# Performance work log

Measured on AMD Instinct MI355X. Metric: run time of the kernel, lower is better.

The kernel has to match this reference:

```python
import jax, jax.numpy as jnp
import numpy as np
import math

B, L, D, H = 2, 2048, 512, 8
DH = D // H  # 64
MAX_SEQ = 2048


def setup_inputs() -> dict:
    key = jax.random.key(0)
    ks = jax.random.split(key, 9)
    rn = lambda k, sh: jax.random.normal(k, sh, dtype=jnp.float32)
    w_scale = 0.02
    # causal mask: 1 where attention is disallowed (upper triangle)
    causal = jnp.triu(jnp.ones((L, L), jnp.float32), k=1)[None, None]
    return {
        "q_in": rn(ks[0], (B, L, D)),
        "k_in": rn(ks[1], (B, L, D)),
        "v_in": rn(ks[2], (B, L, D)),
        "mask": causal,
        "Wq": rn(ks[3], (D, D)) * w_scale,
        "bq": jnp.zeros((D,), jnp.float32),
        "Wk": rn(ks[4], (D, D)) * w_scale,
        "bk": jnp.zeros((D,), jnp.float32),
        "Wv": rn(ks[5], (D, D)) * w_scale,
        "bv": jnp.zeros((D,), jnp.float32),
        "Wfc": rn(ks[6], (D, D)) * w_scale,
        "bfc": jnp.zeros((D,), jnp.float32),
        "E": rn(ks[7], (MAX_SEQ, DH)),  # relative position embedding (non-trainable buffer)
    }


def _heads(x, W, b):
    # [B,L,D] -> [B,H,L,DH]
    y = x @ W + b
    return y.reshape(x.shape[0], x.shape[1], H, DH).transpose(0, 2, 1, 3)


def _qe_mask(len_q):
    # keep[l, m] = (m >= len_q - 1 - l); zeros out invalid relative offsets
    rows = jnp.arange(len_q)[:, None]
    cols = jnp.arange(len_q)[None, :]
    return (cols >= (len_q - 1 - rows)).astype(jnp.float32)


def _skew(QE):
    # Music-Transformer skewing: [B,H,L,M] -> pad left on last dim ->
    # reshape swapping last two dims -> drop first row => Srel [B,H,M,L]
    b, h, l, m = QE.shape
    padded = jnp.pad(QE, ((0, 0), (0, 0), (0, 0), (1, 0)))  # [b,h,l,m+1]
    reshaped = padded.reshape(b, h, m + 1, l)
    return reshaped[:, :, 1:, :]  # [b,h,m,l]


def reference(q_in, k_in, v_in, mask, Wq, bq, Wk, bk, Wv, bv, Wfc, bfc, E):
    q = _heads(q_in, Wq, bq)  # [B,H,L,DH]
    k = _heads(k_in, Wk, bk)
    v = _heads(v_in, Wv, bv)
    len_q = q.shape[2]
    # left embedding slice: E[max(0, MAX_SEQ - len_q):]
    e = E[max(0, MAX_SEQ - len_q):, :]  # [M, DH], M == len_q here
    QE = jnp.einsum('bhld,md->bhlm', q, e)
    QE = QE * _qe_mask(len_q)  # broadcast [L,M] over [B,H,L,M]
    Srel = _skew(QE)  # [B,H,L,L]
    QKt = jnp.einsum('bhld,bhmd->bhlm', q, k)
    logits = (QKt + Srel) / np.sqrt(DH).astype(np.float32)
    logits = logits + mask * (-1e9)
    attn_weights = jax.nn.softmax(logits, axis=-1)
    attn = jnp.einsum('bhlm,bhmd->bhld', attn_weights, v)
    out = attn.transpose(0, 2, 1, 3).reshape(q_in.shape[0], -1, D)
    out = out @ Wfc + bfc
    return out, attn_weights
```

## Files before the change

kernel.cpp:

```cpp
#include <hip/hip_runtime.h>
#include <math.h>

#define L 2048
#define DMODEL 512
#define NH 8
#define DH 64
#define NROWS 4096

typedef __attribute__((ext_vector_type(4))) float f32x4;
typedef __attribute__((ext_vector_type(8))) short s16x8;

#define MFMA(a, b, c) __builtin_amdgcn_mfma_f32_16x16x32_bf16(a, b, c, 0, 0, 0)

static __device__ __forceinline__ ushort f2b(float f) {
    union { float f; unsigned u; } v; v.f = f;
    unsigned r = v.u + 0x7FFF + ((v.u >> 16) & 1);
    return (ushort)(r >> 16);
}

__global__ __launch_bounds__(256)
void cvt_bf16(const float* __restrict__ in, ushort* __restrict__ out, int n8) {
    int i = blockIdx.x * 256 + threadIdx.x;
    if (i < n8) {
        float4 a = *reinterpret_cast<const float4*>(&in[(size_t)i * 8]);
        float4 b = *reinterpret_cast<const float4*>(&in[(size_t)i * 8 + 4]);
        ushort4 o0; o0.x = f2b(a.x); o0.y = f2b(a.y); o0.z = f2b(a.z); o0.w = f2b(a.w);
        ushort4 o1; o1.x = f2b(b.x); o1.y = f2b(b.y); o1.z = f2b(b.z); o1.w = f2b(b.w);
        *reinterpret_cast<ushort4*>(&out[(size_t)i * 8]) = o0;
        *reinterpret_cast<ushort4*>(&out[(size_t)i * 8 + 4]) = o1;
    }
}

__global__ __launch_bounds__(256)
void transpose_w(const float* __restrict__ W0, const float* __restrict__ W1,
                 const float* __restrict__ W2, const float* __restrict__ W3,
                 ushort* __restrict__ T0, ushort* __restrict__ T1,
                 ushort* __restrict__ T2, ushort* __restrict__ T3) {
    const int z = blockIdx.z;
    const float* W = z == 0 ? W0 : (z == 1 ? W1 : (z == 2 ? W2 : W3));
    ushort* T = z == 0 ? T0 : (z == 1 ? T1 : (z == 2 ? T2 : T3));
    __shared__ float Ls[64][65];
    const int tid = threadIdx.x;
    const int k0 = blockIdx.y * 64, n0 = blockIdx.x * 64;
    #pragma unroll
    for (int i = 0; i < 4; ++i) {
        int kk = (tid >> 4) + i * 16, n4 = (tid & 15) * 4;
        float4 v = *reinterpret_cast<const float4*>(&W[(size_t)(k0 + kk) * 512 + n0 + n4]);
        Ls[kk][n4] = v.x; Ls[kk][n4 + 1] = v.y; Ls[kk][n4 + 2] = v.z; Ls[kk][n4 + 3] = v.w;
    }
    __syncthreads();
    #pragma unroll
    for (int i = 0; i < 4; ++i) {
        int nn = (tid >> 4) + i * 16, k4 = (tid & 15) * 4;
        ushort4 o;
        o.x = f2b(Ls[k4 + 0][nn]); o.y = f2b(Ls[k4 + 1][nn]);
        o.z = f2b(Ls[k4 + 2][nn]); o.w = f2b(Ls[k4 + 3][nn]);
        *reinterpret_cast<ushort4*>(&T[(size_t)(n0 + nn) * 512 + k0 + k4]) = o;
    }
}

__global__ __launch_bounds__(256)
void gemm_bf16(const void* __restrict__ A0, const void* __restrict__ A1,
               const void* __restrict__ A2,
               const ushort* __restrict__ W0, const ushort* __restrict__ W1,
               const ushort* __restrict__ W2,
               const float* __restrict__ b0, const float* __restrict__ b1,
               const float* __restrict__ b2,
               void* o0, void* o1, void* o2, int a_f32, int modes) {
    const int z = blockIdx.z;
    const void* A   = z == 0 ? A0 : (z == 1 ? A1 : A2);
    const ushort* Wt = z == 0 ? W0 : (z == 1 ? W1 : W2);
    const float* bias = z == 0 ? b0 : (z == 1 ? b1 : b2);
    void* outp = z == 0 ? o0 : (z == 1 ? o1 : o2);
    const int mode = (modes >> (4 * z)) & 15;

    __shared__ ushort As[128][40];
    __shared__ ushort Bs[64][40];
    const int tid = threadIdx.x;
    const int w = tid >> 6, lane = tid & 63, g = lane >> 4, c = lane & 15;
    const int m0 = blockIdx.y * 128, n0 = blockIdx.x * 64;

    f32x4 acc[2][4];
    #pragma unroll
    for (int rs = 0; rs < 2; ++rs)
        #pragma unroll
        for (int cs = 0; cs < 4; ++cs) acc[rs][cs] = (f32x4){0.f, 0.f, 0.f, 0.f};

    float bsv[4];
    #pragma unroll
    for (int cs = 0; cs < 4; ++cs) bsv[cs] = bias[n0 + 16 * cs + c];

    for (int k0 = 0; k0 < 512; k0 += 32) {
        {
            int row = tid >> 1, kh = (tid & 1) * 16;
            if (a_f32) {
                const float* p = (const float*)A + (size_t)(m0 + row) * 512 + k0 + kh;
                ushort tmp[16];
                #pragma unroll
                for (int q4 = 0; q4 < 4; ++q4) {
                    float4 f = *reinterpret_cast<const float4*>(p + q4 * 4);
                    tmp[q4 * 4 + 0] = f2b(f.x); tmp[q4 * 4 + 1] = f2b(f.y);
                    tmp[q4 * 4 + 2] = f2b(f.z); tmp[q4 * 4 + 3] = f2b(f.w);
                }
                *reinterpret_cast<uint4*>(&As[row][kh]) = *reinterpret_cast<uint4*>(&tmp[0]);
                *reinterpret_cast<uint4*>(&As[row][kh + 8]) = *reinterpret_cast<uint4*>(&tmp[8]);
            } else {
                const ushort* p = (const ushort*)A + (size_t)(m0 + row) * 512 + k0 + kh;
                uint4 x0 = *reinterpret_cast<const uint4*>(p);
                uint4 x1 = *reinterpret_cast<const uint4*>(p + 8);
                *reinterpret_cast<uint4*>(&As[row][kh]) = x0;
                *reinterpret_cast<uint4*>(&As[row][kh + 8]) = x1;
            }
        }
        {
            int n = tid >> 2, kh = (tid & 3) * 8;
            uint4 x = *reinterpret_cast<const uint4*>(&Wt[(size_t)(n0 + n) * 512 + k0 + kh]);
            *reinterpret_cast<uint4*>(&Bs[n][kh]) = x;
        }
        __syncthreads();
        s16x8 af[2], bf[4];
        #pragma unroll
        for (int rs = 0; rs < 2; ++rs)
            af[rs] = *reinterpret_cast<const s16x8*>(&As[32 * w + 16 * rs + c][8 * g]);
        #pragma unroll
        for (int cs = 0; cs < 4; ++cs)
            bf[cs] = *reinterpret_cast<const s16x8*>(&Bs[16 * cs + c][8 * g]);
        #pragma unroll
        for (int rs = 0; rs < 2; ++rs)
            #pragma unroll
            for (int cs = 0; cs < 4; ++cs)
                acc[rs][cs] = MFMA(af[rs], bf[cs], acc[rs][cs]);
        __syncthreads();
    }
    #pragma unroll
    for (int rs = 0; rs < 2; ++rs)
        #pragma unroll
        for (int cs = 0; cs < 4; ++cs)
            #pragma unroll
            for (int r = 0; r < 4; ++r) {
                int row = m0 + 32 * w + 16 * rs + 4 * g + r;
                int n = n0 + 16 * cs + c;
                float v = acc[rs][cs][r] + bsv[cs];
                int bb = row >> 11, l = row & 2047, hh = n >> 6, dh = n & 63;
                if (mode == 0) {
                    ((float*)outp)[(size_t)row * 512 + n] = v;
                } else if (mode == 1) {
                    ((ushort*)outp)[(((size_t)bb * NH + hh) * L + l) * DH + dh] = f2b(v);
                } else {
                    ((ushort*)outp)[(((size_t)bb * NH + hh) * DH + dh) * L + l] = f2b(v);
                }
            }
}

__global__ __launch_bounds__(256, 4)
void attn(const ushort* __restrict__ qws, const ushort* __restrict__ kws,
          const ushort* __restrict__ vtg, const ushort* __restrict__ Ebf,
          float* __restrict__ attnw, ushort* __restrict__ ows) {
    __shared__ float Wsc[4][32][68];
    __shared__ float lred[4][32];
    __shared__ float linvs[32];

    const int tid = threadIdx.x;
    const int w = tid >> 6, lane = tid & 63, g = lane >> 4, c = lane & 15;
    const int bid = blockIdx.x;
    const int bh = bid & 15;
    const int ib = 63 - (bid >> 4);
    const int b = bh >> 3, h = bh & 7;
    const int i0 = ib * 32;
    const int nt = ib + 1;

    const ushort* qb = qws + (size_t)bh * L * DH;
    const ushort* kb = kws + (size_t)bh * L * DH;
    const ushort* vt = vtg + (size_t)bh * DH * L;
    float* ab = attnw + (size_t)bh * L * L;

    float*  Ps = &Wsc[w][0][0];
    ushort* Pw = (ushort*)(Ps + 32 * 36);

    s16x8 aq[2][2];
    #pragma unroll
    for (int rs = 0; rs < 2; ++rs)
        #pragma unroll
        for (int ks = 0; ks < 2; ++ks)
            aq[rs][ks] = *reinterpret_cast<const s16x8*>(
                qb + (size_t)(i0 + 16 * rs + c) * DH + 32 * ks + 8 * g);

    auto computeS = [&](int j0, float (&sv)[2][2][4]) {
        const int rbase = L - 32 - i0 + j0;
        f32x4 TT[4][2];
        #pragma unroll
        for (int ct = 0; ct < 4; ++ct) {
            int rg = rbase + 16 * ct + c;
            rg = rg > L - 1 ? L - 1 : rg;
            s16x8 be0 = *reinterpret_cast<const s16x8*>(Ebf + (size_t)rg * DH + 8 * g);
            s16x8 be1 = *reinterpret_cast<const s16x8*>(Ebf + (size_t)rg * DH + 32 + 8 * g);
            #pragma unroll
            for (int rs = 0; rs < 2; ++rs) {
                f32x4 x = {0.f, 0.f, 0.f, 0.f};
                x = MFMA(aq[rs][0], be0, x);
                x = MFMA(aq[rs][1], be1, x);
                TT[ct][rs] = x;
            }
        }
        float rel[2][2][4];
        #pragma unroll
        for (int r = 0; r < 4; ++r) {
            const int u = c - 4 * g - r;
            const int src = (lane & 48) | ((15 + u) & 15);
            const bool hi = (u >= 1);
            #pragma unroll
            for (int rs = 0; rs < 2; ++rs)
                #pragma unroll
                for (int jh = 0; jh < 2; ++jh) {
                    const int b0 = jh - rs + 1;
                    float va = __shfl(TT[b0][rs][r], src);
                    float vb = __shfl(TT[b0 + 1][rs][r], src);
                    rel[rs][jh][r] = hi ? vb : va;
                }
        }
        s16x8 bk[2][2];
        #pragma unroll
        for (int jh = 0; jh < 2; ++jh)
            #pragma unroll
            for (int ks = 0; ks < 2; ++ks)
                bk[jh][ks] = *reinterpret_cast<const s16x8*>(
                    kb + (size_t)(j0 + 16 * jh + c) * DH + 32 * ks + 8 * g);
        #pragma unroll
        for (int rs = 0; rs < 2; ++rs)
            #pragma unroll
            for (int jh = 0; jh < 2; ++jh) {
                f32x4 x = {0.f, 0.f, 0.f, 0.f};
                x = MFMA(aq[rs][0], bk[jh][0], x);
                x = MFMA(aq[rs][1], bk[jh][1], x);
                #pragma unroll
                for (int r = 0; r < 4; ++r) {
                    const int il = 16 * rs + 4 * g + r;
                    const int jl = 16 * jh + c;
                    float s = (x[r] + rel[rs][jh][r]) * 0.125f;
                    sv[rs][jh][r] = (j0 + jl <= i0 + il) ? s : -1.0e30f;
                }
            }
    };

    float lsum[2][4] = {};
    for (int t = w; t < nt; t += 4) {
        float sv[2][2][4];
        computeS(t * 32, sv);
        #pragma unroll
        for (int rs = 0; rs < 2; ++rs)
            #pragma unroll
            for (int jh = 0; jh < 2; ++jh)
                #pragma unroll
                for (int r = 0; r < 4; ++r)
                    lsum[rs][r] += __expf(sv[rs][jh][r]);
    }
    #pragma unroll
    for (int rs = 0; rs < 2; ++rs)
        #pragma unroll
        for (int r = 0; r < 4; ++r) {
            float s = lsum[rs][r];
            s += __shfl_xor(s, 1); s += __shfl_xor(s, 2);
            s += __shfl_xor(s, 4); s += __shfl_xor(s, 8);
            if (c == 0) lred[w][16 * rs + 4 * g + r] = s;
        }
    __syncthreads();
    if (tid < 32)
        linvs[tid] = 1.0f / (lred[0][tid] + lred[1][tid] + lred[2][tid] + lred[3][tid]);
    __syncthreads();
    float myi[2][4];
    #pragma unroll
    for (int rs = 0; rs < 2; ++rs)
        #pragma unroll
        for (int r = 0; r < 4; ++r)
            myi[rs][r] = linvs[16 * rs + 4 * g + r];

    f32x4 O[2][4];
    #pragma unroll
    for (int rs = 0; rs < 2; ++rs)
        #pragma unroll
        for (int cs = 0; cs < 4; ++cs) O[rs][cs] = (f32x4){0.f, 0.f, 0.f, 0.f};

    for (int t = w; t < nt; t += 4) {
        const int j0 = t * 32;
        float sv[2][2][4];
        computeS(j0, sv);
        #pragma unroll
        for (int rs = 0; rs < 2; ++rs)
            #pragma unroll
            for (int jh = 0; jh < 2; ++jh)
                #pragma unroll
                for (int r = 0; r < 4; ++r) {
                    const int il = 16 * rs + 4 * g + r;
                    const int jl = 16 * jh + c;
                    float p = __expf(sv[rs][jh][r]) * myi[rs][r];
                    Ps[il * 36 + jl] = p;
                    Pw[il * 40 + jl] = f2b(p);
                }
        {
            const int row = lane >> 1, cb = (lane & 1) * 16;
            float* dst = &ab[(size_t)(i0 + row) * L + j0 + cb];
            const float* srcp = &Ps[row * 36 + cb];
            #pragma unroll
            for (int e = 0; e < 4; ++e)
                *reinterpret_cast<float4*>(dst + 4 * e) =
                    *reinterpret_cast<const float4*>(srcp + 4 * e);
        }
        s16x8 pa[2];
        #pragma unroll
        for (int rs2 = 0; rs2 < 2; ++rs2)
            pa[rs2] = *reinterpret_cast<const s16x8*>(&Pw[(16 * rs2 + c) * 40 + 8 * g]);
        #pragma unroll
        for (int cs = 0; cs < 4; ++cs) {
            s16x8 vtb = *reinterpret_cast<const s16x8*>(
                vt + (size_t)(16 * cs + c) * L + j0 + 8 * g);
            #pragma unroll
            for (int rs2 = 0; rs2 < 2; ++rs2)
                O[rs2][cs] = MFMA(pa[rs2], vtb, O[rs2][cs]);
        }
    }

    #pragma unroll
    for (int rs2 = 0; rs2 < 2; ++rs2)
        #pragma unroll
        for (int cs = 0; cs < 4; ++cs)
            #pragma unroll
            for (int r = 0; r < 4; ++r)
                Wsc[w][16 * rs2 + 4 * g + r][16 * cs + c] = O[rs2][cs][r];
    __syncthreads();
    {
        const int i = tid >> 3, d8 = (tid & 7) * 8;
        ushort o[8];
        #pragma unroll
        for (int e = 0; e < 8; ++e) {
            float a = Wsc[0][i][d8 + e] + Wsc[1][i][d8 + e]
                    + Wsc[2][i][d8 + e] + Wsc[3][i][d8 + e];
            o[e] = f2b(a);
        }
        *reinterpret_cast<uint4*>(
            &ows[((size_t)b * L + i0 + i) * DMODEL + h * DH + d8]) =
            *reinterpret_cast<const uint4*>(&o[0]);
    }

    {
        const int row = tid >> 3, cj = (tid & 7) * 4;
        const float4 z = make_float4(0.f, 0.f, 0.f, 0.f);
        float* rowp = &ab[(size_t)(i0 + row) * L];
        for (int j0z = nt * 32; j0z < L; j0z += 32)
            *reinterpret_cast<float4*>(rowp + j0z + cj) = z;
    }
}

extern "C" void kernel_launch(void* const* d_in, const int* in_sizes, int n_in,
                              void* d_out, int out_size, void* d_ws, size_t ws_size,
                              hipStream_t stream) {
    const float* q_in = (const float*)d_in[0];
    const float* k_in = (const float*)d_in[1];
    const float* v_in = (const float*)d_in[2];
    const float* Wq  = (const float*)d_in[4];
    const float* bq  = (const float*)d_in[5];
    const float* Wk  = (const float*)d_in[6];
    const float* bk  = (const float*)d_in[7];
    const float* Wv  = (const float*)d_in[8];
    const float* bv  = (const float*)d_in[9];
    const float* Wfc = (const float*)d_in[10];
    const float* bfc = (const float*)d_in[11];
    const float* E   = (const float*)d_in[12];

    float* out0  = (float*)d_out;
    float* attnw = out0 + (size_t)2 * L * DMODEL;

    const size_t NA = (size_t)NROWS * DMODEL;
    ushort* ws = (ushort*)d_ws;
    ushort* Ebf  = ws;
    ushort* Wqt  = Ebf + (size_t)L * DH;
    ushort* Wkt  = Wqt + 262144;
    ushort* Wvt  = Wkt + 262144;
    ushort* Wfct = Wvt + 262144;
    ushort* qws  = Wfct + 262144;
    ushort* kws  = qws + NA;
    ushort* vtg  = kws + NA;
    ushort* ows  = vtg + NA;

    cvt_bf16<<<dim3(64), 256, 0, stream>>>(E, Ebf, (int)(L * DH / 8));
    transpose_w<<<dim3(8, 8, 4), 256, 0, stream>>>(Wq, Wk, Wv, Wfc, Wqt, Wkt, Wvt, Wfct);
    gemm_bf16<<<dim3(8, 32, 3), 256, 0, stream>>>(q_in, k_in, v_in, Wqt, Wkt, Wvt,
                                                  bq, bk, bv, qws, kws, vtg,
                                                  1, 0x211);
    attn<<<dim3(1024), 256, 0, stream>>>(qws, kws, vtg, Ebf, attnw, ows);
    gemm_bf16<<<dim3(8, 32, 1), 256, 0, stream>>>(ows, ows, ows, Wfct, Wfct, Wfct,
                                                  bfc, bfc, bfc, out0, out0, out0,
                                                  0, 0x0);
}
```

Baseline: 228.4 us.

## Single-pass attention with deferred normalization and paired causal row blocks

The two-pass softmax, which recomputed S to get row sums before writing probabilities, becomes a single pass. Unnormalized exp values go straight to the attention-weight output, and the PV product uses the unnormalized P. A second sweep over each row then rescales the stored weights by 1/rowsum and zeroes the masked part. Each block now has 512 threads (8 waves) and handles a pair of row blocks (i and 63-i) to balance the causal workload. The approach drops the max subtraction, as the original code also did, and adds a global read-modify-write pass over the attention-weight matrix.

```diff
diff --git a/kernel.cpp b/kernel.cpp
--- a/kernel.cpp
+++ b/kernel.cpp
@@ -152,22 +152,20 @@
             }
 }
 
-__global__ __launch_bounds__(256, 4)
+__global__ __launch_bounds__(512, 4)
 void attn(const ushort* __restrict__ qws, const ushort* __restrict__ kws,
           const ushort* __restrict__ vtg, const ushort* __restrict__ Ebf,
           float* __restrict__ attnw, ushort* __restrict__ ows) {
-    __shared__ float Wsc[4][32][68];
-    __shared__ float lred[4][32];
+    __shared__ float Wsc[8][32][68];
+    __shared__ float lred[8][32];
     __shared__ float linvs[32];
 
     const int tid = threadIdx.x;
     const int w = tid >> 6, lane = tid & 63, g = lane >> 4, c = lane & 15;
     const int bid = blockIdx.x;
     const int bh = bid & 15;
-    const int ib = 63 - (bid >> 4);
+    const int pairi = bid >> 4;
     const int b = bh >> 3, h = bh & 7;
-    const int i0 = ib * 32;
-    const int nt = ib + 1;
 
     const ushort* qb = qws + (size_t)bh * L * DH;
     const ushort* kb = kws + (size_t)bh * L * DH;
@@ -177,176 +175,175 @@
     float*  Ps = &Wsc[w][0][0];
     ushort* Pw = (ushort*)(Ps + 32 * 36);
 
-    s16x8 aq[2][2];
-    #pragma unroll
-    for (int rs = 0; rs < 2; ++rs)
-        #pragma unroll
-        for (int ks = 0; ks < 2; ++ks)
-            aq[rs][ks] = *reinterpret_cast<const s16x8*>(
-                qb + (size_t)(i0 + 16 * rs + c) * DH + 32 * ks + 8 * g);
-
-    auto computeS = [&](int j0, float (&sv)[2][2][4]) {
-        const int rbase = L - 32 - i0 + j0;
-        f32x4 TT[4][2];
-        #pragma unroll
-        for (int ct = 0; ct < 4; ++ct) {
-            int rg = rbase + 16 * ct + c;
-            rg = rg > L - 1 ? L - 1 : rg;
-            s16x8 be0 = *reinterpret_cast<const s16x8*>(Ebf + (size_t)rg * DH + 8 * g);
-            s16x8 be1 = *reinterpret_cast<const s16x8*>(Ebf + (size_t)rg * DH + 32 + 8 * g);
-            #pragma unroll
-            for (int rs = 0; rs < 2; ++rs) {
-                f32x4 x = {0.f, 0.f, 0.f, 0.f};
-                x = MFMA(aq[rs][0], be0, x);
-                x = MFMA(aq[rs][1], be1, x);
-                TT[ct][rs] = x;
-            }
-        }
-        float rel[2][2][4];
-        #pragma unroll
-        for (int r = 0; r < 4; ++r) {
-            const int u = c - 4 * g - r;
-            const int src = (lane & 48) | ((15 + u) & 15);
-            const bool hi = (u >= 1);
+    for (int rep = 0; rep < 2; ++rep) {
+        const int ib = rep ? (63 - pairi) : pairi;
+        const int i0 = ib * 32;
+        const int nt = ib + 1;
+        __syncthreads();
+
+        s16x8 aq[2][2];
+        #pragma unroll
+        for (int rs = 0; rs < 2; ++rs)
+            #pragma unroll
+            for (int ks = 0; ks < 2; ++ks)
+                aq[rs][ks] = *reinterpret_cast<const s16x8*>(
+                    qb + (size_t)(i0 + 16 * rs + c) * DH + 32 * ks + 8 * g);
+
+        float lsum[2][4] = {};
+        f32x4 O[2][4];
+        #pragma unroll
+        for (int rs = 0; rs < 2; ++rs)
+            #pragma unroll
+            for (int cs = 0; cs < 4; ++cs) O[rs][cs] = (f32x4){0.f, 0.f, 0.f, 0.f};
+
+        for (int t = w; t < nt; t += 8) {
+            const int j0 = t * 32;
+            const int rbase = L - 32 - i0 + j0;
+            f32x4 TT[4][2];
+            #pragma unroll
+            for (int ct = 0; ct < 4; ++ct) {
+                int rg = rbase + 16 * ct + c;
+                rg = rg > L - 1 ? L - 1 : rg;
+                s16x8 be0 = *reinterpret_cast<const s16x8*>(Ebf + (size_t)rg * DH + 8 * g);
+                s16x8 be1 = *reinterpret_cast<const s16x8*>(Ebf + (size_t)rg * DH + 32 + 8 * g);
+                #pragma unroll
+                for (int rs = 0; rs < 2; ++rs) {
+                    f32x4 x = {0.f, 0.f, 0.f, 0.f};
+                    x = MFMA(aq[rs][0], be0, x);
+                    x = MFMA(aq[rs][1], be1, x);
+                    TT[ct][rs] = x;
+                }
+            }
+            float rel[2][2][4];
+            #pragma unroll
+            for (int r = 0; r < 4; ++r) {
+                const int u = c - 4 * g - r;
+                const int src = (lane & 48) | ((15 + u) & 15);
+                const bool hi = (u >= 1);
+                #pragma unroll
+                for (int rs = 0; rs < 2; ++rs)
+                    #pragma unroll
+                    for (int jh = 0; jh < 2; ++jh) {
+                        const int b0 = jh - rs + 1;
+                        float va = __shfl(TT[b0][rs][r], src);
+                        float vb = __shfl(TT[b0 + 1][rs][r], src);
+                        rel[rs][jh][r] = hi ? vb : va;
+                    }
+            }
+            s16x8 bk[2][2];
+            #pragma unroll
+            for (int jh = 0; jh < 2; ++jh)
+                #pragma unroll
+                for (int ks = 0; ks < 2; ++ks)
+                    bk[jh][ks] = *reinterpret_cast<const s16x8*>(
+                        kb + (size_t)(j0 + 16 * jh + c) * DH + 32 * ks + 8 * g);
             #pragma unroll
             for (int rs = 0; rs < 2; ++rs)
                 #pragma unroll
                 for (int jh = 0; jh < 2; ++jh) {
-                    const int b0 = jh - rs + 1;
-                    float va = __shfl(TT[b0][rs][r], src);
-                    float vb = __shfl(TT[b0 + 1][rs][r], src);
-                    rel[rs][jh][r] = hi ? vb : va;
-                }
-        }
-        s16x8 bk[2][2];
-        #pragma unroll
-        for (int jh = 0; jh < 2; ++jh)
-            #pragma unroll
-            for (int ks = 0; ks < 2; ++ks)
-                bk[jh][ks] = *reinterpret_cast<const s16x8*>(
-                    kb + (size_t)(j0 + 16 * jh + c) * DH + 32 * ks + 8 * g);
-        #pragma unroll
-        for (int rs = 0; rs < 2; ++rs)
-            #pragma unroll
-            for (int jh = 0; jh < 2; ++jh) {
-                f32x4 x = {0.f, 0.f, 0.f, 0.f};
-                x = MFMA(aq[rs][0], bk[jh][0], x);
-                x = MFMA(aq[rs][1], bk[jh][1], x);
-                #pragma unroll
-                for (int r = 0; r < 4; ++r) {
-                    const int il = 16 * rs + 4 * g + r;
-                    const int jl = 16 * jh + c;
-                    float s = (x[r] + rel[rs][jh][r]) * 0.125f;
-                    sv[rs][jh][r] = (j0 + jl <= i0 + il) ? s : -1.0e30f;
-                }
-            }
-    };
-
-    float lsum[2][4] = {};
-    for (int t = w; t < nt; t += 4) {
-        float sv[2][2][4];
-        computeS(t * 32, sv);
-        #pragma unroll
-        for (int rs = 0; rs < 2; ++rs)
-            #pragma unroll
-            for (int jh = 0; jh < 2; ++jh)
+                    f32x4 x = {0.f, 0.f, 0.f, 0.f};
+                    x = MFMA(aq[rs][0], bk[jh][0], x);
+                    x = MFMA(aq[rs][1], bk[jh][1], x);
+                    #pragma unroll
+                    for (int r = 0; r < 4; ++r) {
+                        const int il = 16 * rs + 4 * g + r;
+                        const int jl = 16 * jh + c;
+                        float s = (x[r] + rel[rs][jh][r]) * 0.125f;
+                        float p = (j0 + jl <= i0 + il) ? __expf(s) : 0.0f;
+                        lsum[rs][r] += p;
+                        Ps[il * 36 + jl] = p;
+                        Pw[il * 40 + jl] = f2b(p);
+                    }
+                }
+            {
+                const int row = lane >> 1, cb = (lane & 1) * 16;
+                float* dst = &ab[(size_t)(i0 + row) * L + j0 + cb];
+                const float* srcp = &Ps[row * 36 + cb];
+                #pragma unroll
+                for (int e = 0; e < 4; ++e)
+                    *reinterpret_cast<float4*>(dst + 4 * e) =
+                        *reinterpret_cast<const float4*>(srcp + 4 * e);
+            }
+            s16x8 pa[2];
+            #pragma unroll
+            for (int rs2 = 0; rs2 < 2; ++rs2)
+                pa[rs2] = *reinterpret_cast<const s16x8*>(&Pw[(16 * rs2 + c) * 40 + 8 * g]);
+            #pragma unroll
+            for (int cs = 0; cs < 4; ++cs) {
+                s16x8 vtb = *reinterpret_cast<const s16x8*>(
+                    vt + (size_t)(16 * cs + c) * L + j0 + 8 * g);
+                #pragma unroll
+                for (int rs2 = 0; rs2 < 2; ++rs2)
+                    O[rs2][cs] = MFMA(pa[rs2], vtb, O[rs2][cs]);
+            }
+        }
+
+        #pragma unroll
+        for (int rs = 0; rs < 2; ++rs)
+            #pragma unroll
+            for (int r = 0; r < 4; ++r) {
+                float s = lsum[rs][r];
+                s += __shfl_xor(s, 1); s += __shfl_xor(s, 2);
+                s += __shfl_xor(s, 4); s += __shfl_xor(s, 8);
+                if (c == 0) lred[w][16 * rs + 4 * g + r] = s;
+            }
+        __syncthreads();
+        if (tid < 32) {
+            float l = 0.f;
+            #pragma unroll
+            for (int ww = 0; ww < 8; ++ww) l += lred[ww][tid];
+            linvs[tid] = 1.0f / l;
+        }
+        __syncthreads();
+
+        #pragma unroll
+        for (int rs2 = 0; rs2 < 2; ++rs2)
+            #pragma unroll
+            for (int cs = 0; cs < 4; ++cs)
                 #pragma unroll
                 for (int r = 0; r < 4; ++r)
-                    lsum[rs][r] += __expf(sv[rs][jh][r]);
-    }
-    #pragma unroll
-    for (int rs = 0; rs < 2; ++rs)
-        #pragma unroll
-        for (int r = 0; r < 4; ++r) {
-            float s = lsum[rs][r];
-            s += __shfl_xor(s, 1); s += __shfl_xor(s, 2);
-            s += __shfl_xor(s, 4); s += __shfl_xor(s, 8);
-            if (c == 0) lred[w][16 * rs + 4 * g + r] = s;
-        }
-    __syncthreads();
-    if (tid < 32)
-        linvs[tid] = 1.0f / (lred[0][tid] + lred[1][tid] + lred[2][tid] + lred[3][tid]);
-    __syncthreads();
-    float myi[2][4];
-    #pragma unroll
-    for (int rs = 0; rs < 2; ++rs)
-        #pragma unroll
-        for (int r = 0; r < 4; ++r)
-            myi[rs][r] = linvs[16 * rs + 4 * g + r];
-
-    f32x4 O[2][4];
-    #pragma unroll
-    for (int rs = 0; rs < 2; ++rs)
-        #pragma unroll
-        for (int cs = 0; cs < 4; ++cs) O[rs][cs] = (f32x4){0.f, 0.f, 0.f, 0.f};
-
-    for (int t = w; t < nt; t += 4) {
-        const int j0 = t * 32;
-        float sv[2][2][4];
-        computeS(j0, sv);
-        #pragma unroll
-        for (int rs = 0; rs < 2; ++rs)
-            #pragma unroll
-            for (int jh = 0; jh < 2; ++jh)
-                #pragma unroll
-                for (int r = 0; r < 4; ++r) {
-                    const int il = 16 * rs + 4 * g + r;
-                    const int jl = 16 * jh + c;
-                    float p = __expf(sv[rs][jh][r]) * myi[rs][r];
-                    Ps[il * 36 + jl] = p;
-                    Pw[il * 40 + jl] = f2b(p);
-                }
+                    Wsc[w][16 * rs2 + 4 * g + r][16 * cs + c] = O[rs2][cs][r];
+        __syncthreads();
         {
-            const int row = lane >> 1, cb = (lane & 1) * 16;
-            float* dst = &ab[(size_t)(i0 + row) * L + j0 + cb];
-            const float* srcp = &Ps[row * 36 + cb];
-            #pragma unroll
-            for (int e = 0; e < 4; ++e)
-                *reinterpret_cast<float4*>(dst + 4 * e) =
-                    *reinterpret_cast<const float4*>(srcp + 4 * e);
-        }
-        s16x8 pa[2];
-        #pragma unroll
-        for (int rs2 = 0; rs2 < 2; ++rs2)
-            pa[rs2] = *reinterpret_cast<const s16x8*>(&Pw[(16 * rs2 + c) * 40 + 8 * g]);
-        #pragma unroll
-        for (int cs = 0; cs < 4; ++cs) {
-            s16x8 vtb = *reinterpret_cast<const s16x8*>(
-                vt + (size_t)(16 * cs + c) * L + j0 + 8 * g);
-            #pragma unroll
-            for (int rs2 = 0; rs2 < 2; ++rs2)
-                O[rs2][cs] = MFMA(pa[rs2], vtb, O[rs2][cs]);
-        }
-    }
-
-    #pragma unroll
-    for (int rs2 = 0; rs2 < 2; ++rs2)
-        #pragma unroll
-        for (int cs = 0; cs < 4; ++cs)
-            #pragma unroll
-            for (int r = 0; r < 4; ++r)
-                Wsc[w][16 * rs2 + 4 * g + r][16 * cs + c] = O[rs2][cs][r];
-    __syncthreads();
-    {
-        const int i = tid >> 3, d8 = (tid & 7) * 8;
-        ushort o[8];
-        #pragma unroll
-        for (int e = 0; e < 8; ++e) {
-            float a = Wsc[0][i][d8 + e] + Wsc[1][i][d8 + e]
-                    + Wsc[2][i][d8 + e] + Wsc[3][i][d8 + e];
-            o[e] = f2b(a);
-        }
-        *reinterpret_cast<uint4*>(
-            &ows[((size_t)b * L + i0 + i) * DMODEL + h * DH + d8]) =
-            *reinterpret_cast<const uint4*>(&o[0]);
-    }
-
-    {
-        const int row = tid >> 3, cj = (tid & 7) * 4;
-        const float4 z = make_float4(0.f, 0.f, 0.f, 0.f);
-        float* rowp = &ab[(size_t)(i0 + row) * L];
-        for (int j0z = nt * 32; j0z < L; j0z += 32)
-            *reinterpret_cast<float4*>(rowp + j0z + cj) = z;
+            const int i = tid >> 4, d4 = (tid & 15) * 4;
+            const float inv = linvs[i];
+            ushort o[4];
+            #pragma unroll
+            for (int e = 0; e < 4; ++e) {
+                float a = 0.f;
+                #pragma unroll
+                for (int ww = 0; ww < 8; ++ww) a += Wsc[ww][i][d4 + e];
+                o[e] = f2b(a * inv);
+            }
+            *reinterpret_cast<ushort4*>(
+                &ows[((size_t)b * L + i0 + i) * DMODEL + h * DH + d4]) =
+                *reinterpret_cast<const ushort4*>(&o[0]);
+        }
+
+        {
+            const int r = tid >> 4;
+            const int ig = i0 + r;
+            const float inv = linvs[r];
+            float* rowp = &ab[(size_t)(i0 + r) * L];
+            #pragma unroll 4
+            for (int k = 0; k < 32; ++k) {
+                const int col = (tid & 15) * 4 + k * 64;
+                float4 v;
+                if (col + 3 <= ig) {
+                    v = *reinterpret_cast<const float4*>(rowp + col);
+                    v.x *= inv; v.y *= inv; v.z *= inv; v.w *= inv;
+                } else if (col <= ig) {
+                    v = *reinterpret_cast<const float4*>(rowp + col);
+                    v.x = (col + 0 <= ig) ? v.x * inv : 0.f;
+                    v.y = (col + 1 <= ig) ? v.y * inv : 0.f;
+                    v.z = (col + 2 <= ig) ? v.z * inv : 0.f;
+                    v.w = (col + 3 <= ig) ? v.w * inv : 0.f;
+                } else {
+                    v = make_float4(0.f, 0.f, 0.f, 0.f);
+                }
+                *reinterpret_cast<float4*>(rowp + col) = v;
+            }
+        }
     }
 }
 
@@ -386,7 +383,7 @@
     gemm_bf16<<<dim3(8, 32, 3), 256, 0, stream>>>(q_in, k_in, v_in, Wqt, Wkt, Wvt,
                                                   bq, bk, bv, qws, kws, vtg,
                                                   1, 0x211);
-    attn<<<dim3(1024), 256, 0, stream>>>(qws, kws, vtg, Ebf, attnw, ows);
+    attn<<<dim3(512), 512, 0, stream>>>(qws, kws, vtg, Ebf, attnw, ows);
     gemm_bf16<<<dim3(8, 32, 1), 256, 0, stream>>>(ows, ows, ows, Wfct, Wfct, Wfct,
                                                   bfc, bfc, bfc, out0, out0, out0,
                                                   0, 0x0);
```

Result: slower. 267.1 us (+16.9%).

## Single-pass attention with unnormalized bf16 probabilities and separate rescale kernel

Applied to the files above, without the earlier changes.

Merges the two passes over key tiles (sum pass, then normalize-and-write pass) into one pass. That pass computes exp scores, accumulates row sums and P·V on unnormalized probabilities, and stores them as compact bf16 lower-triangular tiles in workspace. A new rescale kernel then expands these into the full fp32 attention-weight matrix, multiplying by per-row inverse sums and writing zeros with nontemporal stores. This removes the recomputation of QK and the relative-position scores. In exchange it adds an extra workspace round-trip and a kernel launch. Probabilities exported in the attention-weights output now pass through bf16, and exp is taken without max subtraction, as before.

```diff
diff --git a/kernel.cpp b/kernel.cpp
--- a/kernel.cpp
+++ b/kernel.cpp
@@ -16,6 +16,10 @@
     union { float f; unsigned u; } v; v.f = f;
     unsigned r = v.u + 0x7FFF + ((v.u >> 16) & 1);
     return (ushort)(r >> 16);
+}
+static __device__ __forceinline__ float b2f(ushort u) {
+    union { unsigned u; float f; } v; v.u = ((unsigned)u) << 16;
+    return v.f;
 }
 
 __global__ __launch_bounds__(256)
@@ -155,8 +159,9 @@
 __global__ __launch_bounds__(256, 4)
 void attn(const ushort* __restrict__ qws, const ushort* __restrict__ kws,
           const ushort* __restrict__ vtg, const ushort* __restrict__ Ebf,
-          float* __restrict__ attnw, ushort* __restrict__ ows) {
-    __shared__ float Wsc[4][32][68];
+          ushort* __restrict__ pcomp, ushort* __restrict__ ows,
+          float* __restrict__ linvg) {
+    __shared__ ushort PwAll[4][32 * 40];
     __shared__ float lred[4][32];
     __shared__ float linvs[32];
 
@@ -172,10 +177,9 @@
     const ushort* qb = qws + (size_t)bh * L * DH;
     const ushort* kb = kws + (size_t)bh * L * DH;
     const ushort* vt = vtg + (size_t)bh * DH * L;
-    float* ab = attnw + (size_t)bh * L * L;
-
-    float*  Ps = &Wsc[w][0][0];
-    ushort* Pw = (ushort*)(Ps + 32 * 36);
+    ushort* pblk = pcomp + ((size_t)bh * 2080 + (size_t)ib * (ib + 1) / 2) * 1024;
+
+    ushort* Pw = &PwAll[w][0];
 
     s16x8 aq[2][2];
     #pragma unroll
@@ -185,7 +189,15 @@
             aq[rs][ks] = *reinterpret_cast<const s16x8*>(
                 qb + (size_t)(i0 + 16 * rs + c) * DH + 32 * ks + 8 * g);
 
-    auto computeS = [&](int j0, float (&sv)[2][2][4]) {
+    float lsum[2][4] = {};
+    f32x4 O[2][4];
+    #pragma unroll
+    for (int rs = 0; rs < 2; ++rs)
+        #pragma unroll
+        for (int cs = 0; cs < 4; ++cs) O[rs][cs] = (f32x4){0.f, 0.f, 0.f, 0.f};
+
+    for (int t = w; t < nt; t += 4) {
+        const int j0 = t * 32;
         const int rbase = L - 32 - i0 + j0;
         f32x4 TT[4][2];
         #pragma unroll
@@ -237,23 +249,33 @@
                     const int il = 16 * rs + 4 * g + r;
                     const int jl = 16 * jh + c;
                     float s = (x[r] + rel[rs][jh][r]) * 0.125f;
-                    sv[rs][jh][r] = (j0 + jl <= i0 + il) ? s : -1.0e30f;
+                    float p = (j0 + jl <= i0 + il) ? __expf(s) : 0.0f;
+                    lsum[rs][r] += p;
+                    Pw[il * 40 + jl] = f2b(p);
                 }
             }
-    };
-
-    float lsum[2][4] = {};
-    for (int t = w; t < nt; t += 4) {
-        float sv[2][2][4];
-        computeS(t * 32, sv);
-        #pragma unroll
-        for (int rs = 0; rs < 2; ++rs)
-            #pragma unroll
-            for (int jh = 0; jh < 2; ++jh)
-                #pragma unroll
-                for (int r = 0; r < 4; ++r)
-                    lsum[rs][r] += __expf(sv[rs][jh][r]);
-    }
+        {
+            const int row = lane >> 1, cb = (lane & 1) * 16;
+            uint4 x0 = *reinterpret_cast<const uint4*>(&Pw[row * 40 + cb]);
+            uint4 x1 = *reinterpret_cast<const uint4*>(&Pw[row * 40 + cb + 8]);
+            ushort* dst = pblk + (size_t)t * 1024 + lane * 16;
+            *reinterpret_cast<uint4*>(dst) = x0;
+            *reinterpret_cast<uint4*>(dst + 8) = x1;
+        }
+        s16x8 pa[2];
+        #pragma unroll
+        for (int rs2 = 0; rs2 < 2; ++rs2)
+            pa[rs2] = *reinterpret_cast<const s16x8*>(&Pw[(16 * rs2 + c) * 40 + 8 * g]);
+        #pragma unroll
+        for (int cs = 0; cs < 4; ++cs) {
+            s16x8 vtb = *reinterpret_cast<const s16x8*>(
+                vt + (size_t)(16 * cs + c) * L + j0 + 8 * g);
+            #pragma unroll
+            for (int rs2 = 0; rs2 < 2; ++rs2)
+                O[rs2][cs] = MFMA(pa[rs2], vtb, O[rs2][cs]);
+        }
+    }
+
     #pragma unroll
     for (int rs = 0; rs < 2; ++rs)
         #pragma unroll
@@ -264,90 +286,71 @@
             if (c == 0) lred[w][16 * rs + 4 * g + r] = s;
         }
     __syncthreads();
-    if (tid < 32)
-        linvs[tid] = 1.0f / (lred[0][tid] + lred[1][tid] + lred[2][tid] + lred[3][tid]);
+    if (tid < 32) {
+        float l = lred[0][tid] + lred[1][tid] + lred[2][tid] + lred[3][tid];
+        float inv = 1.0f / l;
+        linvs[tid] = inv;
+        linvg[(size_t)bh * L + i0 + tid] = inv;
+    }
     __syncthreads();
-    float myi[2][4];
-    #pragma unroll
-    for (int rs = 0; rs < 2; ++rs)
-        #pragma unroll
-        for (int r = 0; r < 4; ++r)
-            myi[rs][r] = linvs[16 * rs + 4 * g + r];
-
-    f32x4 O[2][4];
-    #pragma unroll
-    for (int rs = 0; rs < 2; ++rs)
-        #pragma unroll
-        for (int cs = 0; cs < 4; ++cs) O[rs][cs] = (f32x4){0.f, 0.f, 0.f, 0.f};
-
-    for (int t = w; t < nt; t += 4) {
-        const int j0 = t * 32;
-        float sv[2][2][4];
-        computeS(j0, sv);
-        #pragma unroll
-        for (int rs = 0; rs < 2; ++rs)
-            #pragma unroll
-            for (int jh = 0; jh < 2; ++jh)
+
+    float (*Obuf)[68] = reinterpret_cast<float(*)[68]>(&PwAll[0][0]);
+    #pragma unroll
+    for (int ww = 0; ww < 4; ++ww) {
+        if (w == ww) {
+            #pragma unroll
+            for (int rs2 = 0; rs2 < 2; ++rs2)
                 #pragma unroll
-                for (int r = 0; r < 4; ++r) {
-                    const int il = 16 * rs + 4 * g + r;
-                    const int jl = 16 * jh + c;
-                    float p = __expf(sv[rs][jh][r]) * myi[rs][r];
-                    Ps[il * 36 + jl] = p;
-                    Pw[il * 40 + jl] = f2b(p);
-                }
-        {
-            const int row = lane >> 1, cb = (lane & 1) * 16;
-            float* dst = &ab[(size_t)(i0 + row) * L + j0 + cb];
-            const float* srcp = &Ps[row * 36 + cb];
-            #pragma unroll
-            for (int e = 0; e < 4; ++e)
-                *reinterpret_cast<float4*>(dst + 4 * e) =
-                    *reinterpret_cast<const float4*>(srcp + 4 * e);
-        }
-        s16x8 pa[2];
-        #pragma unroll
-        for (int rs2 = 0; rs2 < 2; ++rs2)
-            pa[rs2] = *reinterpret_cast<const s16x8*>(&Pw[(16 * rs2 + c) * 40 + 8 * g]);
-        #pragma unroll
-        for (int cs = 0; cs < 4; ++cs) {
-            s16x8 vtb = *reinterpret_cast<const s16x8*>(
-                vt + (size_t)(16 * cs + c) * L + j0 + 8 * g);
-            #pragma unroll
-            for (int rs2 = 0; rs2 < 2; ++rs2)
-                O[rs2][cs] = MFMA(pa[rs2], vtb, O[rs2][cs]);
-        }
-    }
-
-    #pragma unroll
-    for (int rs2 = 0; rs2 < 2; ++rs2)
-        #pragma unroll
-        for (int cs = 0; cs < 4; ++cs)
-            #pragma unroll
-            for (int r = 0; r < 4; ++r)
-                Wsc[w][16 * rs2 + 4 * g + r][16 * cs + c] = O[rs2][cs][r];
-    __syncthreads();
+                for (int cs = 0; cs < 4; ++cs)
+                    #pragma unroll
+                    for (int r = 0; r < 4; ++r) {
+                        const int row = 16 * rs2 + 4 * g + r;
+                        const int col = 16 * cs + c;
+                        if (ww == 0) Obuf[row][col] = O[rs2][cs][r];
+                        else         Obuf[row][col] += O[rs2][cs][r];
+                    }
+        }
+        __syncthreads();
+    }
     {
         const int i = tid >> 3, d8 = (tid & 7) * 8;
+        const float inv = linvs[i];
         ushort o[8];
         #pragma unroll
-        for (int e = 0; e < 8; ++e) {
-            float a = Wsc[0][i][d8 + e] + Wsc[1][i][d8 + e]
-                    + Wsc[2][i][d8 + e] + Wsc[3][i][d8 + e];
-            o[e] = f2b(a);
-        }
+        for (int e = 0; e < 8; ++e) o[e] = f2b(Obuf[i][d8 + e] * inv);
         *reinterpret_cast<uint4*>(
             &ows[((size_t)b * L + i0 + i) * DMODEL + h * DH + d8]) =
             *reinterpret_cast<const uint4*>(&o[0]);
     }
-
-    {
-        const int row = tid >> 3, cj = (tid & 7) * 4;
-        const float4 z = make_float4(0.f, 0.f, 0.f, 0.f);
-        float* rowp = &ab[(size_t)(i0 + row) * L];
-        for (int j0z = nt * 32; j0z < L; j0z += 32)
-            *reinterpret_cast<float4*>(rowp + j0z + cj) = z;
-    }
+}
+
+__global__ __launch_bounds__(256)
+void rescale(const ushort* __restrict__ pcomp, const float* __restrict__ linvg,
+             float* __restrict__ attnw) {
+    const int blk = blockIdx.x;
+    const int bh = blk >> 11, i = blk & 2047;
+    const int ib = i >> 5, r = i & 31;
+    const float inv = linvg[((size_t)bh << 11) + i];
+    const ushort* rowb = pcomp + ((size_t)bh * 2080 + (size_t)ib * (ib + 1) / 2) * 1024 + r * 32;
+    float* dst = attnw + (((size_t)bh << 11) + i) * 2048;
+    const int col0 = threadIdx.x * 8;
+    f32x4 o0 = {0.f, 0.f, 0.f, 0.f}, o1 = {0.f, 0.f, 0.f, 0.f};
+    if (col0 <= i) {
+        const int t = col0 >> 5;
+        const ushort* src = rowb + (size_t)t * 1024 + (col0 & 31);
+        ushort4 u0 = *reinterpret_cast<const ushort4*>(src);
+        ushort4 u1 = *reinterpret_cast<const ushort4*>(src + 4);
+        o0[0] = (col0 + 0 <= i) ? b2f(u0.x) * inv : 0.f;
+        o0[1] = (col0 + 1 <= i) ? b2f(u0.y) * inv : 0.f;
+        o0[2] = (col0 + 2 <= i) ? b2f(u0.z) * inv : 0.f;
+        o0[3] = (col0 + 3 <= i) ? b2f(u0.w) * inv : 0.f;
+        o1[0] = (col0 + 4 <= i) ? b2f(u1.x) * inv : 0.f;
+        o1[1] = (col0 + 5 <= i) ? b2f(u1.y) * inv : 0.f;
+        o1[2] = (col0 + 6 <= i) ? b2f(u1.z) * inv : 0.f;
+        o1[3] = (col0 + 7 <= i) ? b2f(u1.w) * inv : 0.f;
+    }
+    __builtin_nontemporal_store(o0, reinterpret_cast<f32x4*>(dst + col0));
+    __builtin_nontemporal_store(o1, reinterpret_cast<f32x4*>(dst + col0 + 4));
 }
 
 extern "C" void kernel_launch(void* const* d_in, const int* in_sizes, int n_in,
@@ -380,13 +383,16 @@
     ushort* kws  = qws + NA;
     ushort* vtg  = kws + NA;
     ushort* ows  = vtg + NA;
+    float*  linvg = (float*)(ows + NA);
+    ushort* pcomp = (ushort*)(linvg + 32768);
 
     cvt_bf16<<<dim3(64), 256, 0, stream>>>(E, Ebf, (int)(L * DH / 8));
     transpose_w<<<dim3(8, 8, 4), 256, 0, stream>>>(Wq, Wk, Wv, Wfc, Wqt, Wkt, Wvt, Wfct);
     gemm_bf16<<<dim3(8, 32, 3), 256, 0, stream>>>(q_in, k_in, v_in, Wqt, Wkt, Wvt,
                                                   bq, bk, bv, qws, kws, vtg,
                                                   1, 0x211);
-    attn<<<dim3(1024), 256, 0, stream>>>(qws, kws, vtg, Ebf, attnw, ows);
+    attn<<<dim3(1024), 256, 0, stream>>>(qws, kws, vtg, Ebf, pcomp, ows, linvg);
+    rescale<<<dim3(32768), 256, 0, stream>>>(pcomp, linvg, attnw);
     gemm_bf16<<<dim3(8, 32, 1), 256, 0, stream>>>(ows, ows, ows, Wfct, Wfct, Wfct,
                                                   bfc, bfc, bfc, out0, out0, out0,
                                                   0, 0x0);
```

Measured after the change: 237.9 us. +4.2%, slower.
